# Kernel tuning notes

Measured on AMD Instinct MI355X. Metric: run time of the kernel, lower is better.

The kernel has to match this reference:

```python
import jax, jax.numpy as jnp
import numpy as np

D_MODEL = 1024
D_STATE = 16
D_CONV = 4
EXPAND = 2
MLP_EXPAND = 2
D_INNER = EXPAND * D_MODEL          # 2048
DT_RANK = (D_MODEL + 15) // 16      # 64
BATCH, SEQ = 2, 1024


def setup_inputs() -> dict:
    key = jax.random.key(0)
    ks = jax.random.split(key, 16)
    s = 0.02
    inp = {
        "x": jax.random.normal(ks[0], (BATCH, SEQ, D_MODEL), jnp.float32),
        "norm1_g": jnp.ones((D_MODEL,), jnp.float32),
        "norm1_b": jnp.zeros((D_MODEL,), jnp.float32),
        "in_proj_w": jax.random.normal(ks[1], (2 * D_INNER, D_MODEL), jnp.float32) * s,
        "conv_w": jax.random.normal(ks[2], (D_INNER, 1, D_CONV), jnp.float32) * s,
        "conv_b": jnp.zeros((D_INNER,), jnp.float32),
        "x_proj_w": jax.random.normal(ks[3], (DT_RANK + 2 * D_STATE, D_INNER), jnp.float32) * s,
        "dt_proj_w": jax.random.normal(ks[4], (D_INNER, DT_RANK), jnp.float32) * s,
        "dt_proj_b": jax.random.normal(ks[5], (D_INNER,), jnp.float32) * 0.1,
        "A_log": jnp.log(jnp.broadcast_to(jnp.arange(1, D_STATE + 1, dtype=jnp.float32), (D_INNER, D_STATE))),
        "D_param": jnp.ones((D_INNER,), jnp.float32),
        "out_proj_w": jax.random.normal(ks[6], (D_MODEL, D_INNER), jnp.float32) * s,
        "norm2_g": jnp.ones((D_MODEL,), jnp.float32),
        "norm2_b": jnp.zeros((D_MODEL,), jnp.float32),
        "mlp_w1": jax.random.normal(ks[7], (MLP_EXPAND * D_MODEL, D_MODEL), jnp.float32) * s,
        "mlp_b1": jnp.zeros((MLP_EXPAND * D_MODEL,), jnp.float32),
        "mlp_w2": jax.random.normal(ks[8], (D_MODEL, MLP_EXPAND * D_MODEL), jnp.float32) * s,
        "mlp_b2": jnp.zeros((D_MODEL,), jnp.float32),
    }
    return inp


def _layernorm(x, g, b, eps=1e-5):
    m = jnp.mean(x, axis=-1, keepdims=True)
    v = jnp.var(x, axis=-1, keepdims=True)
    return (x - m) * jax.lax.rsqrt(v + eps) * g + b


def _silu(x):
    return x * jax.nn.sigmoid(x)


def _mamba(x, in_proj_w, conv_w, conv_b, x_proj_w, dt_proj_w, dt_proj_b, A_log, D_param, out_proj_w):
    # x: (B, L, d_model)
    xz = x @ in_proj_w.T                              # (B, L, 2*Di)
    xc, z = jnp.split(xz, 2, axis=-1)                 # each (B, L, Di)
    # causal depthwise conv over time
    xc_t = xc.transpose(0, 2, 1)                      # (B, Di, L)
    xc_t = jax.lax.conv_general_dilated(
        xc_t, conv_w, window_strides=(1,), padding=[(D_CONV - 1, 0)],
        dimension_numbers=("NCH", "OIH", "NCH"), feature_group_count=D_INNER,
    ) + conv_b[None, :, None]
    xc = _silu(xc_t).transpose(0, 2, 1)               # (B, L, Di)

    dbc = xc @ x_proj_w.T                             # (B, L, dt_rank + 2N)
    dt, Bm, Cm = jnp.split(dbc, [DT_RANK, DT_RANK + D_STATE], axis=-1)
    dt = jax.nn.softplus(dt @ dt_proj_w.T + dt_proj_b)  # (B, L, Di)
    A = -jnp.exp(A_log)                               # (Di, N)

    def step(h, inp):
        dt_t, B_t, C_t, x_t = inp                     # (B,Di),(B,N),(B,N),(B,Di)
        dA = jnp.exp(dt_t[..., None] * A)             # (B, Di, N)
        h = dA * h + (dt_t * x_t)[..., None] * B_t[:, None, :]
        y = jnp.einsum("bdn,bn->bd", h, C_t)
        return h, y

    h0 = jnp.zeros((x.shape[0], D_INNER, D_STATE), x.dtype)
    xs = (dt.transpose(1, 0, 2), Bm.transpose(1, 0, 2), Cm.transpose(1, 0, 2), xc.transpose(1, 0, 2))
    _, ys = jax.lax.scan(step, h0, xs)                # ys: (L, B, Di)
    y = ys.transpose(1, 0, 2) + xc * D_param          # skip term D*x
    y = y * _silu(z)
    return y @ out_proj_w.T                           # (B, L, d_model)


def reference(x, norm1_g, norm1_b, in_proj_w, conv_w, conv_b, x_proj_w, dt_proj_w,
              dt_proj_b, A_log, D_param, out_proj_w, norm2_g, norm2_b,
              mlp_w1, mlp_b1, mlp_w2, mlp_b2):
    # residual + Mamba(LN(x))  (droppath=0 -> identity)
    h = x + _mamba(_layernorm(x, norm1_g, norm1_b), in_proj_w, conv_w, conv_b,
                   x_proj_w, dt_proj_w, dt_proj_b, A_log, D_param, out_proj_w)
    # residual + MLP(LN(h))    (dropout eval -> identity)
    m = _layernorm(h, norm2_g, norm2_b)
    m = jax.nn.gelu(m @ mlp_w1.T + mlp_b1, approximate=False) @ mlp_w2.T + mlp_b2
    return h + m
```

## Files before the change

### kernel.cpp

```cpp
#include <hip/hip_runtime.h>
#include <math.h>

#define D_MODEL 1024
#define D_INNER 2048
#define DT_RANK 64
#define D_STATE 16
#define NBC 96
#define BATCH 2
#define SEQ 1024
#define TOK (BATCH*SEQ)
#define CS 32
#define NCH 32
#define XKSPLIT 16

typedef __attribute__((ext_vector_type(8))) short short8;
typedef __attribute__((ext_vector_type(4))) float f32x4;

__device__ __forceinline__ float softplus_f(float x) {
    return (x > 20.0f) ? x : log1pf(__expf(x));
}
__device__ __forceinline__ float gelu_f(float x) {
    return 0.5f * x * (1.0f + erff(x * 0.70710678118654752f));
}
__device__ __forceinline__ float silu_f(float x) {
    return x / (1.0f + __expf(-x));
}
__device__ __forceinline__ ushort f2bf(float f) {
    unsigned u = __float_as_uint(f);
    unsigned r = (u + 0x7fffu + ((u >> 16) & 1u)) >> 16;
    return (ushort)r;
}
__device__ __forceinline__ float bf2f(ushort u) {
    return __uint_as_float(((unsigned)u) << 16);
}

__global__ void convert_weights_kernel(const float* __restrict__ Wp, const float* __restrict__ Wo,
                                       const float* __restrict__ W1, const float* __restrict__ W2,
                                       const float* __restrict__ Wx, const float* __restrict__ Wdt,
                                       ushort* __restrict__ Wpb, ushort* __restrict__ Wob,
                                       ushort* __restrict__ W1b, ushort* __restrict__ W2b,
                                       ushort* __restrict__ Wxb, ushort* __restrict__ Wdtb) {
    int i = blockIdx.x * 256 + threadIdx.x;
    const float* src; ushort* dst; int off;
    if      (i < 1048576) { src = Wp;  dst = Wpb;  off = i; }
    else if (i < 1572864) { src = Wo;  dst = Wob;  off = i - 1048576; }
    else if (i < 2097152) { src = W1;  dst = W1b;  off = i - 1572864; }
    else if (i < 2621440) { src = W2;  dst = W2b;  off = i - 2097152; }
    else if (i < 2670592) { src = Wx;  dst = Wxb;  off = i - 2621440; }
    else if (i < 2703360) { src = Wdt; dst = Wdtb; off = i - 2670592; }
    else return;
    float4 v = ((const float4*)src)[off];
    ushort4 o;
    o.x = f2bf(v.x); o.y = f2bf(v.y); o.z = f2bf(v.z); o.w = f2bf(v.w);
    ((ushort4*)dst)[off] = o;
}

__global__ void ln_bf16_kernel(const float* __restrict__ x, const float* __restrict__ g,
                               const float* __restrict__ b, ushort* __restrict__ out) {
    int row = blockIdx.x;
    const float* xr = x + (size_t)row * D_MODEL;
    ushort* outr = out + (size_t)row * D_MODEL;
    int tid = threadIdx.x;
    float4 v = ((const float4*)xr)[tid];
    float s  = v.x + v.y + v.z + v.w;
    float sq = v.x*v.x + v.y*v.y + v.z*v.z + v.w*v.w;
    #pragma unroll
    for (int o = 32; o > 0; o >>= 1) {
        s  += __shfl_down(s,  o);
        sq += __shfl_down(sq, o);
    }
    __shared__ float ss[4], ssq[4];
    int wid = tid >> 6, lane = tid & 63;
    if (lane == 0) { ss[wid] = s; ssq[wid] = sq; }
    __syncthreads();
    if (tid == 0) {
        float a = 0.f, c = 0.f;
        for (int i = 0; i < 4; i++) { a += ss[i]; c += ssq[i]; }
        ss[0] = a; ssq[0] = c;
    }
    __syncthreads();
    float mean = ss[0] * (1.0f / D_MODEL);
    float var  = ssq[0] * (1.0f / D_MODEL) - mean * mean;
    float rstd = rsqrtf(var + 1e-5f);
    float4 gg = ((const float4*)g)[tid];
    float4 bb = ((const float4*)b)[tid];
    ushort4 o;
    o.x = f2bf((v.x - mean) * rstd * gg.x + bb.x);
    o.y = f2bf((v.y - mean) * rstd * gg.y + bb.y);
    o.z = f2bf((v.z - mean) * rstd * gg.z + bb.z);
    o.w = f2bf((v.w - mean) * rstd * gg.w + bb.w);
    ((ushort4*)outr)[tid] = o;
}

template<int BM, int BN, int ACT, bool BIAS, bool RES, bool OUTBF>
__global__ __launch_bounds__(256)
void mfma_gemm(const ushort* __restrict__ A, const ushort* __restrict__ W,
               const float* __restrict__ bias,
               const float* __restrict__ res, int ldr,
               void* __restrict__ Cout, int ldc, int K) {
    constexpr int WM = BM / 2, WN = BN / 2, FM = WM / 16, FN = WN / 16;
    __shared__ __align__(16) ushort As[BM * 32];
    __shared__ __align__(16) ushort Ws[BN * 32];
    const int tid  = threadIdx.x;
    const int lane = tid & 63, w = tid >> 6;
    const int wr = w >> 1, wc = w & 1;
    const int row0 = blockIdx.y * BM, col0 = blockIdx.x * BN;
    const int l16 = lane >> 4, l15 = lane & 15;
    const int srow = tid >> 2;
    const int scol = (tid & 3) * 8;

    f32x4 acc[FM][FN] = {};

    for (int k0 = 0; k0 < K; k0 += 32) {
        #pragma unroll
        for (int s = 0; s < BM / 64; s++) {
            const ushort* g = A + (size_t)(row0 + s * 64 + srow) * K + k0 + scol;
            __builtin_amdgcn_global_load_lds(
                (const __attribute__((address_space(1))) void*)g,
                (__attribute__((address_space(3))) void*)((char*)As + s * 4096 + w * 1024),
                16, 0, 0);
        }
        #pragma unroll
        for (int s = 0; s < BN / 64; s++) {
            const ushort* g = W + (size_t)(col0 + s * 64 + srow) * K + k0 + scol;
            __builtin_amdgcn_global_load_lds(
                (const __attribute__((address_space(1))) void*)g,
                (__attribute__((address_space(3))) void*)((char*)Ws + s * 4096 + w * 1024),
                16, 0, 0);
        }
        __syncthreads();

        short8 a[FM], b[FN];
        #pragma unroll
        for (int m = 0; m < FM; m++)
            a[m] = *(const short8*)(As + (wr * WM + m * 16 + l15) * 32 + l16 * 8);
        #pragma unroll
        for (int n = 0; n < FN; n++)
            b[n] = *(const short8*)(Ws + (wc * WN + n * 16 + l15) * 32 + l16 * 8);
        #pragma unroll
        for (int m = 0; m < FM; m++)
            #pragma unroll
            for (int n = 0; n < FN; n++)
                acc[m][n] = __builtin_amdgcn_mfma_f32_16x16x32_bf16(a[m], b[n], acc[m][n], 0, 0, 0);
        __syncthreads();
    }

    #pragma unroll
    for (int m = 0; m < FM; m++) {
        const int r0 = row0 + wr * WM + m * 16 + l16 * 4;
        #pragma unroll
        for (int n = 0; n < FN; n++) {
            const int c = col0 + wc * WN + n * 16 + l15;
            const float bv = BIAS ? bias[c] : 0.f;
            #pragma unroll
            for (int q = 0; q < 4; q++) {
                const int r = r0 + q;
                float v = acc[m][n][q] + bv;
                if (ACT == 1) v = softplus_f(v);
                else if (ACT == 2) v = gelu_f(v);
                if (RES) v += res[(size_t)r * ldr + c];
                if (OUTBF) ((ushort*)Cout)[(size_t)r * ldc + c] = f2bf(v);
                else       ((float*)Cout)[(size_t)r * ldc + c] = v;
            }
        }
    }
}

__global__ __launch_bounds__(256)
void xproj_split_kernel(const ushort* __restrict__ A,
                        const ushort* __restrict__ W,
                        float* __restrict__ part) {
    __shared__ __align__(16) ushort As[128 * 64];
    __shared__ __align__(16) ushort Bs[96 * 64];
    const int tid = threadIdx.x;
    const int lane = tid & 63, w = tid >> 6;
    const int l16 = lane >> 4, l15 = lane & 15;
    const int kbase = blockIdx.x * (D_INNER / XKSPLIT);
    const int row0 = blockIdx.y * 128;
    const int srow = tid >> 3;
    const int scol = (tid & 7) * 8;

    f32x4 acc[2][6] = {};

    for (int k0 = 0; k0 < D_INNER / XKSPLIT; k0 += 64) {
        #pragma unroll
        for (int s = 0; s < 4; s++) {
            const ushort* g = A + (size_t)(row0 + s * 32 + srow) * D_INNER + kbase + k0 + scol;
            __builtin_amdgcn_global_load_lds(
                (const __attribute__((address_space(1))) void*)g,
                (__attribute__((address_space(3))) void*)((char*)As + s * 4096 + w * 1024),
                16, 0, 0);
        }
        #pragma unroll
        for (int s = 0; s < 3; s++) {
            const ushort* g = W + (size_t)(s * 32 + srow) * D_INNER + kbase + k0 + scol;
            __builtin_amdgcn_global_load_lds(
                (const __attribute__((address_space(1))) void*)g,
                (__attribute__((address_space(3))) void*)((char*)Bs + s * 4096 + w * 1024),
                16, 0, 0);
        }
        __syncthreads();
        #pragma unroll
        for (int ks = 0; ks < 2; ks++) {
            short8 a[2], b[6];
            #pragma unroll
            for (int m = 0; m < 2; m++)
                a[m] = *(const short8*)(As + (w * 32 + m * 16 + l15) * 64 + ks * 32 + l16 * 8);
            #pragma unroll
            for (int n = 0; n < 6; n++)
                b[n] = *(const short8*)(Bs + (n * 16 + l15) * 64 + ks * 32 + l16 * 8);
            #pragma unroll
            for (int m = 0; m < 2; m++)
                #pragma unroll
                for (int n = 0; n < 6; n++)
                    acc[m][n] = __builtin_amdgcn_mfma_f32_16x16x32_bf16(a[m], b[n], acc[m][n], 0, 0, 0);
        }
        __syncthreads();
    }

    float* p = part + (size_t)blockIdx.x * D_INNER * NBC;
    #pragma unroll
    for (int m = 0; m < 2; m++) {
        const int r0 = row0 + w * 32 + m * 16 + l16 * 4;
        #pragma unroll
        for (int n = 0; n < 6; n++) {
            const int c = n * 16 + l15;
            #pragma unroll
            for (int q = 0; q < 4; q++)
                p[(size_t)(r0 + q) * NBC + c] = acc[m][n][q];
        }
    }
}

__global__ void xproj_reduce_kernel(const float* __restrict__ part,
                                    float* __restrict__ dbc, ushort* __restrict__ dtin_b) {
    int i = blockIdx.x * 256 + threadIdx.x;
    if (i >= D_INNER * NBC) return;
    float s = 0.f;
    #pragma unroll
    for (int k = 0; k < XKSPLIT; k++) s += part[(size_t)k * D_INNER * NBC + i];
    dbc[i] = s;
    int r = i / NBC, c = i - r * NBC;
    if (c < DT_RANK) dtin_b[r * DT_RANK + c] = f2bf(s);
}

__global__ void conv_silu_kernel(const ushort* __restrict__ xzb, const float* __restrict__ cw,
                                 const float* __restrict__ cb, ushort* __restrict__ xcb) {
    int idx = blockIdx.x * 256 + threadIdx.x;
    int c  = idx & (D_INNER - 1);
    int bt = idx >> 11;
    int b  = bt >> 10;
    int t  = bt & (SEQ - 1);
    float acc = cb[c];
    #pragma unroll
    for (int j = 0; j < 4; j++) {
        int tt = t - 3 + j;
        if (tt >= 0) acc += cw[c*4 + j] * bf2f(xzb[((size_t)(b*SEQ + tt)) * 4096 + c]);
    }
    xcb[idx] = f2bf(silu_f(acc));
}

__global__ void scan_chunk_kernel(const float* __restrict__ dt, const float* __restrict__ dbc,
                                  const ushort* __restrict__ xcb, const float* __restrict__ A_log,
                                  float* __restrict__ chunkA, float* __restrict__ chunkH) {
    int idx = blockIdx.x * 256 + threadIdx.x;
    int ng = idx & 3;
    int d  = (idx >> 2) & (D_INNER - 1);
    int r  = idx >> 13;
    int c  = r & (NCH - 1);
    int b  = r >> 5;
    const int nb = ng * 4;
    float Arow[4];
    #pragma unroll
    for (int j = 0; j < 4; j++) Arow[j] = -__expf(A_log[d * D_STATE + nb + j]);
    float h[4] = {};
    float ap[4] = {1.f, 1.f, 1.f, 1.f};
    const size_t rbase = (size_t)(b * SEQ + c * CS);
    for (int t = 0; t < CS; t++) {
        size_t row = rbase + t;
        float dtv = dt[row * D_INNER + d];
        float xv  = bf2f(xcb[row * D_INNER + d]);
        const float* bc = dbc + row * NBC + DT_RANK;
        float dtx = dtv * xv;
        #pragma unroll
        for (int j = 0; j < 4; j++) {
            float dA = __expf(dtv * Arow[j]);
            ap[j] *= dA;
            h[j] = dA * h[j] + dtx * bc[nb + j];
        }
    }
    size_t obase = ((size_t)(b * NCH + c) * D_STATE + nb) * D_INNER + d;
    #pragma unroll
    for (int j = 0; j < 4; j++) {
        chunkA[obase + (size_t)j * D_INNER] = ap[j];
        chunkH[obase + (size_t)j * D_INNER] = h[j];
    }
}

__global__ void scan_combine_kernel(const float* __restrict__ chunkA, float* __restrict__ chunkH) {
    int idx = blockIdx.x * 256 + threadIdx.x;
    int d = idx & (D_INNER - 1);
    int r = idx >> 11;
    int n = r & (D_STATE - 1);
    int b = r >> 4;
    float h = 0.f;
    for (int c = 0; c < NCH; c++) {
        size_t o = ((size_t)((b * NCH + c) * D_STATE + n)) * D_INNER + d;
        float a  = chunkA[o];
        float hl = chunkH[o];
        chunkH[o] = h;
        h = a * h + hl;
    }
}

__global__ void scan_final_kernel(const float* __restrict__ dt, const float* __restrict__ dbc,
                                  const ushort* __restrict__ xcb, const float* __restrict__ A_log,
                                  const float* __restrict__ chunkH, const ushort* __restrict__ xzb,
                                  const float* __restrict__ Dp, ushort* __restrict__ yb) {
    int idx = blockIdx.x * 256 + threadIdx.x;
    int ng = idx & 3;
    int d  = (idx >> 2) & (D_INNER - 1);
    int r  = idx >> 13;
    int c  = r & (NCH - 1);
    int b  = r >> 5;
    const int nb = ng * 4;
    float Arow[4];
    #pragma unroll
    for (int j = 0; j < 4; j++) Arow[j] = -__expf(A_log[d * D_STATE + nb + j]);
    float h[4];
    size_t obase = ((size_t)(b * NCH + c) * D_STATE + nb) * D_INNER + d;
    #pragma unroll
    for (int j = 0; j < 4; j++) h[j] = chunkH[obase + (size_t)j * D_INNER];
    const float Dpv = Dp[d];
    const size_t rbase = (size_t)(b * SEQ + c * CS);
    for (int t = 0; t < CS; t++) {
        size_t row = rbase + t;
        float dtv = dt[row * D_INNER + d];
        float xv  = bf2f(xcb[row * D_INNER + d]);
        const float* bc = dbc + row * NBC + DT_RANK;
        float dtx = dtv * xv;
        float yv = 0.f;
        #pragma unroll
        for (int j = 0; j < 4; j++) {
            float dA = __expf(dtv * Arow[j]);
            h[j] = dA * h[j] + dtx * bc[nb + j];
            yv += h[j] * bc[D_STATE + nb + j];
        }
        yv += __shfl_xor(yv, 1);
        yv += __shfl_xor(yv, 2);
        if (ng == 0) {
            float z = bf2f(xzb[row * 4096 + 2048 + d]);
            yb[row * D_INNER + d] = f2bf((yv + xv * Dpv) * silu_f(z));
        }
    }
}

extern "C" void kernel_launch(void* const* d_in, const int* in_sizes, int n_in,
                              void* d_out, int out_size, void* d_ws, size_t ws_size,
                              hipStream_t stream) {
    const float* x    = (const float*)d_in[0];
    const float* n1g  = (const float*)d_in[1];
    const float* n1b  = (const float*)d_in[2];
    const float* Wp   = (const float*)d_in[3];
    const float* cw   = (const float*)d_in[4];
    const float* cb   = (const float*)d_in[5];
    const float* Wx   = (const float*)d_in[6];
    const float* Wdt  = (const float*)d_in[7];
    const float* bdt  = (const float*)d_in[8];
    const float* Alog = (const float*)d_in[9];
    const float* Dp   = (const float*)d_in[10];
    const float* Wo   = (const float*)d_in[11];
    const float* n2g  = (const float*)d_in[12];
    const float* n2b  = (const float*)d_in[13];
    const float* W1   = (const float*)d_in[14];
    const float* b1   = (const float*)d_in[15];
    const float* W2   = (const float*)d_in[16];
    const float* b2   = (const float*)d_in[17];
    float* out = (float*)d_out;
    float* ws  = (float*)d_ws;

    const size_t M1 = 1024 * 1024;
    ushort* xzb   = (ushort*)ws;
    ushort* xcb   = (ushort*)(ws + 8*M1);
    float*  dtb   = ws + 10*M1;
    float*  part  = ws + 14*M1;
    float*  hbuf  = ws + 14*M1;
    float*  dbc   = ws + 18*M1;
    ushort* dtin_b= (ushort*)(ws + 18*M1 + 262144);
    ushort* xnb   = (ushort*)(ws + 18*M1 + 524288);
    ushort* mb    = xnb;
    ushort* yb    = (ushort*)(ws + 20*M1);
    ushort* t1b   = yb;
    ushort* Wpb   = (ushort*)(ws + 22*M1);
    float*  chunkA= ws + 22*M1;
    ushort* Wob   = (ushort*)(ws + 24*M1);
    ushort* W1b   = (ushort*)(ws + 25*M1);
    ushort* W2b   = (ushort*)(ws + 26*M1);
    ushort* Wxb   = (ushort*)(ws + 27*M1);
    ushort* Wdtb  = (ushort*)(ws + 27*M1 + 131072);
    float*  chunkH = out;

    convert_weights_kernel<<<(2703360 + 255)/256, 256, 0, stream>>>(
        Wp, Wo, W1, W2, Wx, Wdt, Wpb, Wob, W1b, W2b, Wxb, Wdtb);

    ln_bf16_kernel<<<TOK, 256, 0, stream>>>(x, n1g, n1b, xnb);
    mfma_gemm<128,128,0,false,false,true><<<dim3(4096/128, 2048/128), 256, 0, stream>>>(
        xnb, Wpb, nullptr, nullptr, 0, xzb, 2*D_INNER, D_MODEL);
    conv_silu_kernel<<<TOK*D_INNER/256, 256, 0, stream>>>(xzb, cw, cb, xcb);
    xproj_split_kernel<<<dim3(XKSPLIT, 2048/128), 256, 0, stream>>>(xcb, Wxb, part);
    xproj_reduce_kernel<<<(D_INNER*NBC + 255)/256, 256, 0, stream>>>(part, dbc, dtin_b);
    mfma_gemm<128,128,1,true,false,false><<<dim3(2048/128, 2048/128), 256, 0, stream>>>(
        dtin_b, Wdtb, bdt, nullptr, 0, dtb, D_INNER, DT_RANK);
    scan_chunk_kernel<<<BATCH*NCH*D_INNER*4/256, 256, 0, stream>>>(dtb, dbc, xcb, Alog, chunkA, chunkH);
    scan_combine_kernel<<<BATCH*D_STATE*D_INNER/256, 256, 0, stream>>>(chunkA, chunkH);
    scan_final_kernel<<<BATCH*NCH*D_INNER*4/256, 256, 0, stream>>>(dtb, dbc, xcb, Alog, chunkH,
                                                                   xzb, Dp, yb);
    mfma_gemm<128,64,0,false,true,false><<<dim3(1024/64, 2048/128), 256, 0, stream>>>(
        yb, Wob, nullptr, x, D_MODEL, hbuf, D_MODEL, D_INNER);
    ln_bf16_kernel<<<TOK, 256, 0, stream>>>(hbuf, n2g, n2b, mb);
    mfma_gemm<128,128,2,true,false,true><<<dim3(2048/128, 2048/128), 256, 0, stream>>>(
        mb, W1b, b1, nullptr, 0, t1b, D_INNER, D_MODEL);
    mfma_gemm<128,64,0,true,true,false><<<dim3(1024/64, 2048/128), 256, 0, stream>>>(
        t1b, W2b, b2, hbuf, D_MODEL, out, D_MODEL, D_INNER);
}
```

Measured before the change: 270.3 us.

## Store scan inputs time-major per channel for vectorized contiguous scan loads

Switches the scan operands (dt, B/C, conv output, z, y) to a channel-major, time-contiguous layout. GEMM epilogues write dt and z transposed, xproj partials are written transposed, and two bf16 transpose kernels convert xc and y between layouts. The scan kernels then load four timesteps at once as vectors instead of strided per-token loads. The cost is two extra transpose passes and scattered transposed stores in the GEMM epilogues.

New measurement: 340.8 us. +26.1%, slower.

```diff
diff --git a/kernel.cpp b/kernel.cpp
--- a/kernel.cpp
+++ b/kernel.cpp
@@ -15,6 +15,7 @@
 
 typedef __attribute__((ext_vector_type(8))) short short8;
 typedef __attribute__((ext_vector_type(4))) float f32x4;
+typedef __attribute__((ext_vector_type(4))) unsigned short us4;
 
 __device__ __forceinline__ float softplus_f(float x) {
     return (x > 20.0f) ? x : log1pf(__expf(x));
@@ -92,12 +93,12 @@
     ((ushort4*)outr)[tid] = o;
 }
 
-template<int BM, int BN, int ACT, bool BIAS, bool RES, bool OUTBF>
+template<int BM, int BN, int ACT, bool BIAS, bool RES, int OUTMODE>
 __global__ __launch_bounds__(256)
 void mfma_gemm(const ushort* __restrict__ A, const ushort* __restrict__ W,
                const float* __restrict__ bias,
                const float* __restrict__ res, int ldr,
-               void* __restrict__ Cout, int ldc, int K) {
+               void* __restrict__ Cout, void* __restrict__ Cout2, int ldc, int K) {
     constexpr int WM = BM / 2, WN = BN / 2, FM = WM / 16, FN = WN / 16;
     __shared__ __align__(16) ushort As[BM * 32];
     __shared__ __align__(16) ushort Ws[BN * 32];
@@ -152,15 +153,34 @@
         for (int n = 0; n < FN; n++) {
             const int c = col0 + wc * WN + n * 16 + l15;
             const float bv = BIAS ? bias[c] : 0.f;
+            float v[4];
             #pragma unroll
             for (int q = 0; q < 4; q++) {
-                const int r = r0 + q;
-                float v = acc[m][n][q] + bv;
-                if (ACT == 1) v = softplus_f(v);
-                else if (ACT == 2) v = gelu_f(v);
-                if (RES) v += res[(size_t)r * ldr + c];
-                if (OUTBF) ((ushort*)Cout)[(size_t)r * ldc + c] = f2bf(v);
-                else       ((float*)Cout)[(size_t)r * ldc + c] = v;
+                v[q] = acc[m][n][q] + bv;
+                if (ACT == 1) v[q] = softplus_f(v[q]);
+                else if (ACT == 2) v[q] = gelu_f(v[q]);
+                if (RES) v[q] += res[(size_t)(r0 + q) * ldr + c];
+            }
+            if (OUTMODE == 0) {
+                #pragma unroll
+                for (int q = 0; q < 4; q++)
+                    ((float*)Cout)[(size_t)(r0 + q) * ldc + c] = v[q];
+            } else if (OUTMODE == 1) {
+                #pragma unroll
+                for (int q = 0; q < 4; q++)
+                    ((ushort*)Cout)[(size_t)(r0 + q) * ldc + c] = f2bf(v[q]);
+            } else if (OUTMODE == 2) {
+                f32x4 p; p[0] = v[0]; p[1] = v[1]; p[2] = v[2]; p[3] = v[3];
+                *(f32x4*)((float*)Cout + (size_t)c * ldc + r0) = p;
+            } else {
+                if (c < D_INNER) {
+                    #pragma unroll
+                    for (int q = 0; q < 4; q++)
+                        ((ushort*)Cout)[(size_t)(r0 + q) * D_INNER + c] = f2bf(v[q]);
+                } else {
+                    us4 p; p[0] = f2bf(v[0]); p[1] = f2bf(v[1]); p[2] = f2bf(v[2]); p[3] = f2bf(v[3]);
+                    *(us4*)((ushort*)Cout2 + (size_t)(c - D_INNER) * TOK + r0) = p;
+                }
             }
         }
     }
@@ -218,33 +238,31 @@
         __syncthreads();
     }
 
-    float* p = part + (size_t)blockIdx.x * D_INNER * NBC;
+    float* p = part + (size_t)blockIdx.x * NBC * TOK;
     #pragma unroll
     for (int m = 0; m < 2; m++) {
         const int r0 = row0 + w * 32 + m * 16 + l16 * 4;
         #pragma unroll
         for (int n = 0; n < 6; n++) {
             const int c = n * 16 + l15;
-            #pragma unroll
-            for (int q = 0; q < 4; q++)
-                p[(size_t)(r0 + q) * NBC + c] = acc[m][n][q];
+            *(f32x4*)(p + (size_t)c * TOK + r0) = acc[m][n];
         }
     }
 }
 
 __global__ void xproj_reduce_kernel(const float* __restrict__ part,
-                                    float* __restrict__ dbc, ushort* __restrict__ dtin_b) {
+                                    float* __restrict__ dbcT, ushort* __restrict__ dtin_b) {
     int i = blockIdx.x * 256 + threadIdx.x;
-    if (i >= D_INNER * NBC) return;
+    if (i >= NBC * TOK) return;
     float s = 0.f;
     #pragma unroll
-    for (int k = 0; k < XKSPLIT; k++) s += part[(size_t)k * D_INNER * NBC + i];
-    dbc[i] = s;
-    int r = i / NBC, c = i - r * NBC;
-    if (c < DT_RANK) dtin_b[r * DT_RANK + c] = f2bf(s);
-}
-
-__global__ void conv_silu_kernel(const ushort* __restrict__ xzb, const float* __restrict__ cw,
+    for (int k = 0; k < XKSPLIT; k++) s += part[(size_t)k * NBC * TOK + i];
+    dbcT[i] = s;
+    int n = i >> 11, row = i & (TOK - 1);
+    if (n < DT_RANK) dtin_b[row * DT_RANK + n] = f2bf(s);
+}
+
+__global__ void conv_silu_kernel(const ushort* __restrict__ xprec, const float* __restrict__ cw,
                                  const float* __restrict__ cb, ushort* __restrict__ xcb) {
     int idx = blockIdx.x * 256 + threadIdx.x;
     int c  = idx & (D_INNER - 1);
@@ -255,13 +273,31 @@
     #pragma unroll
     for (int j = 0; j < 4; j++) {
         int tt = t - 3 + j;
-        if (tt >= 0) acc += cw[c*4 + j] * bf2f(xzb[((size_t)(b*SEQ + tt)) * 4096 + c]);
+        if (tt >= 0) acc += cw[c*4 + j] * bf2f(xprec[((size_t)(b*SEQ + tt)) * D_INNER + c]);
     }
     xcb[idx] = f2bf(silu_f(acc));
 }
 
-__global__ void scan_chunk_kernel(const float* __restrict__ dt, const float* __restrict__ dbc,
-                                  const ushort* __restrict__ xcb, const float* __restrict__ A_log,
+__global__ __launch_bounds__(256)
+void transpose_bf16_kernel(const ushort* __restrict__ in, ushort* __restrict__ out) {
+    __shared__ ushort tile[64][68];
+    const int tx = threadIdx.x & 63, ty = threadIdx.x >> 6;
+    const int r0 = blockIdx.y * 64, c0 = blockIdx.x * 64;
+    #pragma unroll
+    for (int i = 0; i < 16; i++) {
+        int rr = ty * 16 + i;
+        tile[rr][tx] = in[(size_t)(r0 + rr) * TOK + c0 + tx];
+    }
+    __syncthreads();
+    #pragma unroll
+    for (int i = 0; i < 16; i++) {
+        int rr = ty * 16 + i;
+        out[(size_t)(c0 + rr) * TOK + r0 + tx] = tile[tx][rr];
+    }
+}
+
+__global__ void scan_chunk_kernel(const float* __restrict__ dtT, const float* __restrict__ dbcT,
+                                  const ushort* __restrict__ xcbT, const float* __restrict__ A_log,
                                   float* __restrict__ chunkA, float* __restrict__ chunkH) {
     int idx = blockIdx.x * 256 + threadIdx.x;
     int ng = idx & 3;
@@ -273,20 +309,29 @@
     float Arow[4];
     #pragma unroll
     for (int j = 0; j < 4; j++) Arow[j] = -__expf(A_log[d * D_STATE + nb + j]);
+    const int rbase = b * SEQ + c * CS;
+    const float*  pdt = dtT  + (size_t)d * TOK + rbase;
+    const ushort* pxv = xcbT + (size_t)d * TOK + rbase;
+    const float*  pB  = dbcT + (size_t)(DT_RANK + nb) * TOK + rbase;
+    const float*  pC  = dbcT + (size_t)(DT_RANK + D_STATE + nb) * TOK + rbase;
     float h[4] = {};
     float ap[4] = {1.f, 1.f, 1.f, 1.f};
-    const size_t rbase = (size_t)(b * SEQ + c * CS);
-    for (int t = 0; t < CS; t++) {
-        size_t row = rbase + t;
-        float dtv = dt[row * D_INNER + d];
-        float xv  = bf2f(xcb[row * D_INNER + d]);
-        const float* bc = dbc + row * NBC + DT_RANK;
-        float dtx = dtv * xv;
-        #pragma unroll
-        for (int j = 0; j < 4; j++) {
-            float dA = __expf(dtv * Arow[j]);
-            ap[j] *= dA;
-            h[j] = dA * h[j] + dtx * bc[nb + j];
+    for (int it = 0; it < CS / 4; ++it) {
+        f32x4 dt4 = *(const f32x4*)(pdt + it * 4);
+        us4   xu  = *(const us4*)(pxv + it * 4);
+        f32x4 Bv[4];
+        #pragma unroll
+        for (int j = 0; j < 4; j++) Bv[j] = *(const f32x4*)(pB + (size_t)j * TOK + it * 4);
+        #pragma unroll
+        for (int q = 0; q < 4; ++q) {
+            float dtv = dt4[q];
+            float dtx = dtv * bf2f(xu[q]);
+            #pragma unroll
+            for (int j = 0; j < 4; j++) {
+                float dA = __expf(dtv * Arow[j]);
+                ap[j] *= dA;
+                h[j] = dA * h[j] + dtx * Bv[j][q];
+            }
         }
     }
     size_t obase = ((size_t)(b * NCH + c) * D_STATE + nb) * D_INNER + d;
@@ -313,10 +358,10 @@
     }
 }
 
-__global__ void scan_final_kernel(const float* __restrict__ dt, const float* __restrict__ dbc,
-                                  const ushort* __restrict__ xcb, const float* __restrict__ A_log,
-                                  const float* __restrict__ chunkH, const ushort* __restrict__ xzb,
-                                  const float* __restrict__ Dp, ushort* __restrict__ yb) {
+__global__ void scan_final_kernel(const float* __restrict__ dtT, const float* __restrict__ dbcT,
+                                  const ushort* __restrict__ xcbT, const float* __restrict__ A_log,
+                                  const float* __restrict__ chunkH, const ushort* __restrict__ zT,
+                                  const float* __restrict__ Dp, ushort* __restrict__ ybT) {
     int idx = blockIdx.x * 256 + threadIdx.x;
     int ng = idx & 3;
     int d  = (idx >> 2) & (D_INNER - 1);
@@ -332,25 +377,50 @@
     #pragma unroll
     for (int j = 0; j < 4; j++) h[j] = chunkH[obase + (size_t)j * D_INNER];
     const float Dpv = Dp[d];
-    const size_t rbase = (size_t)(b * SEQ + c * CS);
-    for (int t = 0; t < CS; t++) {
-        size_t row = rbase + t;
-        float dtv = dt[row * D_INNER + d];
-        float xv  = bf2f(xcb[row * D_INNER + d]);
-        const float* bc = dbc + row * NBC + DT_RANK;
-        float dtx = dtv * xv;
-        float yv = 0.f;
+    const int rbase = b * SEQ + c * CS;
+    const float*  pdt = dtT  + (size_t)d * TOK + rbase;
+    const ushort* pxv = xcbT + (size_t)d * TOK + rbase;
+    const ushort* pz  = zT   + (size_t)d * TOK + rbase;
+    const float*  pB  = dbcT + (size_t)(DT_RANK + nb) * TOK + rbase;
+    const float*  pC  = dbcT + (size_t)(DT_RANK + D_STATE + nb) * TOK + rbase;
+    ushort*       py  = ybT  + (size_t)d * TOK + rbase;
+    for (int it = 0; it < CS / 4; ++it) {
+        f32x4 dt4 = *(const f32x4*)(pdt + it * 4);
+        us4   xu  = *(const us4*)(pxv + it * 4);
+        f32x4 Bv[4], Cv[4];
         #pragma unroll
         for (int j = 0; j < 4; j++) {
-            float dA = __expf(dtv * Arow[j]);
-            h[j] = dA * h[j] + dtx * bc[nb + j];
-            yv += h[j] * bc[D_STATE + nb + j];
-        }
-        yv += __shfl_xor(yv, 1);
-        yv += __shfl_xor(yv, 2);
+            Bv[j] = *(const f32x4*)(pB + (size_t)j * TOK + it * 4);
+            Cv[j] = *(const f32x4*)(pC + (size_t)j * TOK + it * 4);
+        }
+        float yv4[4];
+        #pragma unroll
+        for (int q = 0; q < 4; ++q) {
+            float dtv = dt4[q];
+            float dtx = dtv * bf2f(xu[q]);
+            float yv = 0.f;
+            #pragma unroll
+            for (int j = 0; j < 4; j++) {
+                float dA = __expf(dtv * Arow[j]);
+                h[j] = dA * h[j] + dtx * Bv[j][q];
+                yv += h[j] * Cv[j][q];
+            }
+            yv4[q] = yv;
+        }
+        #pragma unroll
+        for (int q = 0; q < 4; ++q) {
+            yv4[q] += __shfl_xor(yv4[q], 1);
+            yv4[q] += __shfl_xor(yv4[q], 2);
+        }
         if (ng == 0) {
-            float z = bf2f(xzb[row * 4096 + 2048 + d]);
-            yb[row * D_INNER + d] = f2bf((yv + xv * Dpv) * silu_f(z));
+            us4 zu = *(const us4*)(pz + it * 4);
+            us4 o;
+            #pragma unroll
+            for (int q = 0; q < 4; ++q) {
+                float z = bf2f(zu[q]);
+                o[q] = f2bf((yv4[q] + bf2f(xu[q]) * Dpv) * silu_f(z));
+            }
+            *(us4*)(py + it * 4) = o;
         }
     }
 }
@@ -380,46 +450,51 @@
     float* ws  = (float*)d_ws;
 
     const size_t M1 = 1024 * 1024;
-    ushort* xzb   = (ushort*)ws;
-    ushort* xcb   = (ushort*)(ws + 8*M1);
-    float*  dtb   = ws + 10*M1;
-    float*  part  = ws + 14*M1;
-    float*  hbuf  = ws + 14*M1;
-    float*  dbc   = ws + 18*M1;
-    ushort* dtin_b= (ushort*)(ws + 18*M1 + 262144);
-    ushort* xnb   = (ushort*)(ws + 18*M1 + 524288);
+    ushort* xprec = (ushort*)ws;
+    ushort* zT    = (ushort*)(ws + 2*M1);
+    ushort* xcb   = (ushort*)(ws + 4*M1);
+    ushort* xcbT  = (ushort*)(ws + 6*M1);
+    float*  dtT   = ws + 8*M1;
+    float*  part  = ws + 12*M1;
+    float*  hbuf  = ws + 12*M1;
+    float*  dbcT  = ws + 15*M1;
+    ushort* dtin_b= (ushort*)(ws + 15*M1 + 262144);
+    ushort* xnb   = (ushort*)(ws + 15*M1 + 524288);
     ushort* mb    = xnb;
-    ushort* yb    = (ushort*)(ws + 20*M1);
+    ushort* ybT   = (ushort*)(ws + 17*M1);
+    ushort* yb    = (ushort*)(ws + 19*M1);
     ushort* t1b   = yb;
-    ushort* Wpb   = (ushort*)(ws + 22*M1);
-    float*  chunkA= ws + 22*M1;
-    ushort* Wob   = (ushort*)(ws + 24*M1);
-    ushort* W1b   = (ushort*)(ws + 25*M1);
-    ushort* W2b   = (ushort*)(ws + 26*M1);
-    ushort* Wxb   = (ushort*)(ws + 27*M1);
-    ushort* Wdtb  = (ushort*)(ws + 27*M1 + 131072);
+    ushort* Wpb   = (ushort*)(ws + 21*M1);
+    float*  chunkA= ws + 21*M1;
+    ushort* Wob   = (ushort*)(ws + 23*M1);
+    ushort* W1b   = (ushort*)(ws + 24*M1);
+    ushort* W2b   = (ushort*)(ws + 25*M1);
+    ushort* Wxb   = (ushort*)(ws + 26*M1);
+    ushort* Wdtb  = (ushort*)(ws + 26*M1 + 131072);
     float*  chunkH = out;
 
     convert_weights_kernel<<<(2703360 + 255)/256, 256, 0, stream>>>(
         Wp, Wo, W1, W2, Wx, Wdt, Wpb, Wob, W1b, W2b, Wxb, Wdtb);
 
     ln_bf16_kernel<<<TOK, 256, 0, stream>>>(x, n1g, n1b, xnb);
-    mfma_gemm<128,128,0,false,false,true><<<dim3(4096/128, 2048/128), 256, 0, stream>>>(
-        xnb, Wpb, nullptr, nullptr, 0, xzb, 2*D_INNER, D_MODEL);
-    conv_silu_kernel<<<TOK*D_INNER/256, 256, 0, stream>>>(xzb, cw, cb, xcb);
+    mfma_gemm<128,128,0,false,false,3><<<dim3(4096/128, 2048/128), 256, 0, stream>>>(
+        xnb, Wpb, nullptr, nullptr, 0, xprec, zT, D_INNER, D_MODEL);
+    conv_silu_kernel<<<TOK*D_INNER/256, 256, 0, stream>>>(xprec, cw, cb, xcb);
+    transpose_bf16_kernel<<<dim3(32,32), 256, 0, stream>>>(xcb, xcbT);
     xproj_split_kernel<<<dim3(XKSPLIT, 2048/128), 256, 0, stream>>>(xcb, Wxb, part);
-    xproj_reduce_kernel<<<(D_INNER*NBC + 255)/256, 256, 0, stream>>>(part, dbc, dtin_b);
-    mfma_gemm<128,128,1,true,false,false><<<dim3(2048/128, 2048/128), 256, 0, stream>>>(
-        dtin_b, Wdtb, bdt, nullptr, 0, dtb, D_INNER, DT_RANK);
-    scan_chunk_kernel<<<BATCH*NCH*D_INNER*4/256, 256, 0, stream>>>(dtb, dbc, xcb, Alog, chunkA, chunkH);
+    xproj_reduce_kernel<<<(NBC*TOK + 255)/256, 256, 0, stream>>>(part, dbcT, dtin_b);
+    mfma_gemm<128,128,1,true,false,2><<<dim3(2048/128, 2048/128), 256, 0, stream>>>(
+        dtin_b, Wdtb, bdt, nullptr, 0, dtT, nullptr, TOK, DT_RANK);
+    scan_chunk_kernel<<<BATCH*NCH*D_INNER*4/256, 256, 0, stream>>>(dtT, dbcT, xcbT, Alog, chunkA, chunkH);
     scan_combine_kernel<<<BATCH*D_STATE*D_INNER/256, 256, 0, stream>>>(chunkA, chunkH);
-    scan_final_kernel<<<BATCH*NCH*D_INNER*4/256, 256, 0, stream>>>(dtb, dbc, xcb, Alog, chunkH,
-                                                                   xzb, Dp, yb);
-    mfma_gemm<128,64,0,false,true,false><<<dim3(1024/64, 2048/128), 256, 0, stream>>>(
-        yb, Wob, nullptr, x, D_MODEL, hbuf, D_MODEL, D_INNER);
+    scan_final_kernel<<<BATCH*NCH*D_INNER*4/256, 256, 0, stream>>>(dtT, dbcT, xcbT, Alog, chunkH,
+                                                                   zT, Dp, ybT);
+    transpose_bf16_kernel<<<dim3(32,32), 256, 0, stream>>>(ybT, yb);
+    mfma_gemm<128,64,0,false,true,0><<<dim3(1024/64, 2048/128), 256, 0, stream>>>(
+        yb, Wob, nullptr, x, D_MODEL, hbuf, nullptr, D_MODEL, D_INNER);
     ln_bf16_kernel<<<TOK, 256, 0, stream>>>(hbuf, n2g, n2b, mb);
-    mfma_gemm<128,128,2,true,false,true><<<dim3(2048/128, 2048/128), 256, 0, stream>>>(
-        mb, W1b, b1, nullptr, 0, t1b, D_INNER, D_MODEL);
-    mfma_gemm<128,64,0,true,true,false><<<dim3(1024/64, 2048/128), 256, 0, stream>>>(
-        t1b, W2b, b2, hbuf, D_MODEL, out, D_MODEL, D_INNER);
-}
+    mfma_gemm<128,128,2,true,false,1><<<dim3(2048/128, 2048/128), 256, 0, stream>>>(
+        mb, W1b, b1, nullptr, 0, t1b, nullptr, D_INNER, D_MODEL);
+    mfma_gemm<128,64,0,true,true,0><<<dim3(1024/64, 2048/128), 256, 0, stream>>>(
+        t1b, W2b, b2, hbuf, D_MODEL, out, nullptr, D_MODEL, D_INNER);
+}
```

## Stage scan chunk inputs in LDS and batch per-timestep loads and stores

Applied to the files above, without the earlier changes.

The chunk scan and final scan kernels now have each block cooperatively load a 64-channel by 32-timestep tile of dt, x, z and the B/C values into shared memory. Each thread then reads its time series from LDS as 4-wide vectors, and the final kernel stages its bf16 outputs in LDS and writes them back row-coalesced. Before, each thread issued serial global loads every timestep with poor coalescing (stride of 4 lanes per channel) and repeatedly read B/C. The cost is extra shared memory, a block barrier, and padded LDS layouts that may cause bank conflicts.

Result: no change. 267.3 us (-1.1%).

```diff
diff --git a/kernel.cpp b/kernel.cpp
--- a/kernel.cpp
+++ b/kernel.cpp
@@ -15,6 +15,7 @@
 
 typedef __attribute__((ext_vector_type(8))) short short8;
 typedef __attribute__((ext_vector_type(4))) float f32x4;
+typedef __attribute__((ext_vector_type(4))) unsigned short us4;
 
 __device__ __forceinline__ float softplus_f(float x) {
     return (x > 20.0f) ? x : log1pf(__expf(x));
@@ -260,36 +261,61 @@
     xcb[idx] = f2bf(silu_f(acc));
 }
 
-__global__ void scan_chunk_kernel(const float* __restrict__ dt, const float* __restrict__ dbc,
-                                  const ushort* __restrict__ xcb, const float* __restrict__ A_log,
-                                  float* __restrict__ chunkA, float* __restrict__ chunkH) {
-    int idx = blockIdx.x * 256 + threadIdx.x;
-    int ng = idx & 3;
-    int d  = (idx >> 2) & (D_INNER - 1);
-    int r  = idx >> 13;
-    int c  = r & (NCH - 1);
-    int b  = r >> 5;
-    const int nb = ng * 4;
+__global__ __launch_bounds__(256)
+void scan_chunk_kernel(const float* __restrict__ dtb, const float* __restrict__ dbc,
+                       const ushort* __restrict__ xcb, const float* __restrict__ A_log,
+                       float* __restrict__ chunkA, float* __restrict__ chunkH) {
+    __shared__ float  dtS[64][36];
+    __shared__ ushort xS[64][36];
+    __shared__ float  BS[16][36];
+    const int bid = blockIdx.x;
+    const int dg = bid & 31, cc = (bid >> 5) & 31, b = bid >> 10;
+    const int d0 = dg * 64;
+    const int tid = threadIdx.x, lane = tid & 63, wv = tid >> 6;
+    const int rbase = b * SEQ + cc * CS;
+
+    #pragma unroll
+    for (int k = 0; k < 8; k++) {
+        int tt = k * 4 + wv;
+        size_t row = (size_t)(rbase + tt);
+        dtS[lane][tt] = dtb[row * D_INNER + d0 + lane];
+        xS[lane][tt]  = xcb[row * D_INNER + d0 + lane];
+    }
+    #pragma unroll
+    for (int k = 0; k < 2; k++) {
+        int ii = k * 256 + tid;
+        int val = ii & 15, tt = ii >> 4;
+        BS[val][tt] = dbc[(size_t)(rbase + tt) * NBC + DT_RANK + val];
+    }
+    __syncthreads();
+
+    const int d_local = tid >> 2, ng = tid & 3, nb = ng * 4;
+    const int d = d0 + d_local;
     float Arow[4];
     #pragma unroll
     for (int j = 0; j < 4; j++) Arow[j] = -__expf(A_log[d * D_STATE + nb + j]);
     float h[4] = {};
     float ap[4] = {1.f, 1.f, 1.f, 1.f};
-    const size_t rbase = (size_t)(b * SEQ + c * CS);
-    for (int t = 0; t < CS; t++) {
-        size_t row = rbase + t;
-        float dtv = dt[row * D_INNER + d];
-        float xv  = bf2f(xcb[row * D_INNER + d]);
-        const float* bc = dbc + row * NBC + DT_RANK;
-        float dtx = dtv * xv;
-        #pragma unroll
-        for (int j = 0; j < 4; j++) {
-            float dA = __expf(dtv * Arow[j]);
-            ap[j] *= dA;
-            h[j] = dA * h[j] + dtx * bc[nb + j];
-        }
-    }
-    size_t obase = ((size_t)(b * NCH + c) * D_STATE + nb) * D_INNER + d;
+    #pragma unroll
+    for (int it = 0; it < 8; ++it) {
+        f32x4 dt4 = *(const f32x4*)&dtS[d_local][it * 4];
+        us4   xu  = *(const us4*)&xS[d_local][it * 4];
+        f32x4 Bv[4];
+        #pragma unroll
+        for (int j = 0; j < 4; j++) Bv[j] = *(const f32x4*)&BS[nb + j][it * 4];
+        #pragma unroll
+        for (int q = 0; q < 4; ++q) {
+            float dtv = dt4[q];
+            float dtx = dtv * bf2f(xu[q]);
+            #pragma unroll
+            for (int j = 0; j < 4; j++) {
+                float dA = __expf(dtv * Arow[j]);
+                ap[j] *= dA;
+                h[j] = dA * h[j] + dtx * Bv[j][q];
+            }
+        }
+    }
+    size_t obase = ((size_t)((b * NCH + cc) * D_STATE) + nb) * D_INNER + d;
     #pragma unroll
     for (int j = 0; j < 4; j++) {
         chunkA[obase + (size_t)j * D_INNER] = ap[j];
@@ -313,45 +339,98 @@
     }
 }
 
-__global__ void scan_final_kernel(const float* __restrict__ dt, const float* __restrict__ dbc,
-                                  const ushort* __restrict__ xcb, const float* __restrict__ A_log,
-                                  const float* __restrict__ chunkH, const ushort* __restrict__ xzb,
-                                  const float* __restrict__ Dp, ushort* __restrict__ yb) {
-    int idx = blockIdx.x * 256 + threadIdx.x;
-    int ng = idx & 3;
-    int d  = (idx >> 2) & (D_INNER - 1);
-    int r  = idx >> 13;
-    int c  = r & (NCH - 1);
-    int b  = r >> 5;
-    const int nb = ng * 4;
+__global__ __launch_bounds__(256)
+void scan_final_kernel(const float* __restrict__ dtb, const float* __restrict__ dbc,
+                       const ushort* __restrict__ xcb, const float* __restrict__ A_log,
+                       const float* __restrict__ chunkH, const ushort* __restrict__ xzb,
+                       const float* __restrict__ Dp, ushort* __restrict__ yb) {
+    __shared__ float  dtS[64][36];
+    __shared__ ushort xS[64][36];
+    __shared__ ushort zS[64][36];
+    __shared__ float  BS[16][36];
+    __shared__ float  CSld[16][36];
+    __shared__ ushort ySt[64][36];
+    const int bid = blockIdx.x;
+    const int dg = bid & 31, cc = (bid >> 5) & 31, b = bid >> 10;
+    const int d0 = dg * 64;
+    const int tid = threadIdx.x, lane = tid & 63, wv = tid >> 6;
+    const int rbase = b * SEQ + cc * CS;
+
+    #pragma unroll
+    for (int k = 0; k < 8; k++) {
+        int tt = k * 4 + wv;
+        size_t row = (size_t)(rbase + tt);
+        dtS[lane][tt] = dtb[row * D_INNER + d0 + lane];
+        xS[lane][tt]  = xcb[row * D_INNER + d0 + lane];
+        zS[lane][tt]  = xzb[row * 4096 + 2048 + d0 + lane];
+    }
+    #pragma unroll
+    for (int k = 0; k < 4; k++) {
+        int ii = k * 256 + tid;
+        int val = ii & 31, tt = ii >> 5;
+        float v = dbc[(size_t)(rbase + tt) * NBC + DT_RANK + val];
+        if (val < 16) BS[val][tt] = v;
+        else          CSld[val - 16][tt] = v;
+    }
+    __syncthreads();
+
+    const int d_local = tid >> 2, ng = tid & 3, nb = ng * 4;
+    const int d = d0 + d_local;
     float Arow[4];
     #pragma unroll
     for (int j = 0; j < 4; j++) Arow[j] = -__expf(A_log[d * D_STATE + nb + j]);
     float h[4];
-    size_t obase = ((size_t)(b * NCH + c) * D_STATE + nb) * D_INNER + d;
+    size_t obase = ((size_t)((b * NCH + cc) * D_STATE) + nb) * D_INNER + d;
     #pragma unroll
     for (int j = 0; j < 4; j++) h[j] = chunkH[obase + (size_t)j * D_INNER];
     const float Dpv = Dp[d];
-    const size_t rbase = (size_t)(b * SEQ + c * CS);
-    for (int t = 0; t < CS; t++) {
-        size_t row = rbase + t;
-        float dtv = dt[row * D_INNER + d];
-        float xv  = bf2f(xcb[row * D_INNER + d]);
-        const float* bc = dbc + row * NBC + DT_RANK;
-        float dtx = dtv * xv;
-        float yv = 0.f;
+
+    #pragma unroll
+    for (int it = 0; it < 8; ++it) {
+        f32x4 dt4 = *(const f32x4*)&dtS[d_local][it * 4];
+        us4   xu  = *(const us4*)&xS[d_local][it * 4];
+        f32x4 Bv[4], Cv[4];
         #pragma unroll
         for (int j = 0; j < 4; j++) {
-            float dA = __expf(dtv * Arow[j]);
-            h[j] = dA * h[j] + dtx * bc[nb + j];
-            yv += h[j] * bc[D_STATE + nb + j];
-        }
-        yv += __shfl_xor(yv, 1);
-        yv += __shfl_xor(yv, 2);
+            Bv[j] = *(const f32x4*)&BS[nb + j][it * 4];
+            Cv[j] = *(const f32x4*)&CSld[nb + j][it * 4];
+        }
+        float yv4[4];
+        #pragma unroll
+        for (int q = 0; q < 4; ++q) {
+            float dtv = dt4[q];
+            float dtx = dtv * bf2f(xu[q]);
+            float yv = 0.f;
+            #pragma unroll
+            for (int j = 0; j < 4; j++) {
+                float dA = __expf(dtv * Arow[j]);
+                h[j] = dA * h[j] + dtx * Bv[j][q];
+                yv += h[j] * Cv[j][q];
+            }
+            yv4[q] = yv;
+        }
+        #pragma unroll
+        for (int q = 0; q < 4; ++q) {
+            yv4[q] += __shfl_xor(yv4[q], 1);
+            yv4[q] += __shfl_xor(yv4[q], 2);
+        }
         if (ng == 0) {
-            float z = bf2f(xzb[row * 4096 + 2048 + d]);
-            yb[row * D_INNER + d] = f2bf((yv + xv * Dpv) * silu_f(z));
-        }
+            us4 zu = *(const us4*)&zS[d_local][it * 4];
+            us4 xo = *(const us4*)&xS[d_local][it * 4];
+            us4 o;
+            #pragma unroll
+            for (int q = 0; q < 4; ++q) {
+                float z = bf2f(zu[q]);
+                o[q] = f2bf((yv4[q] + bf2f(xo[q]) * Dpv) * silu_f(z));
+            }
+            *(us4*)&ySt[d_local][it * 4] = o;
+        }
+    }
+    __syncthreads();
+    #pragma unroll
+    for (int k = 0; k < 8; k++) {
+        int tt = k * 4 + wv;
+        yb[(size_t)(rbase + tt) * D_INNER + d0 + lane] = ySt[lane][tt];
     }
 }
 
@@ -411,10 +490,10 @@
     xproj_reduce_kernel<<<(D_INNER*NBC + 255)/256, 256, 0, stream>>>(part, dbc, dtin_b);
     mfma_gemm<128,128,1,true,false,false><<<dim3(2048/128, 2048/128), 256, 0, stream>>>(
         dtin_b, Wdtb, bdt, nullptr, 0, dtb, D_INNER, DT_RANK);
-    scan_chunk_kernel<<<BATCH*NCH*D_INNER*4/256, 256, 0, stream>>>(dtb, dbc, xcb, Alog, chunkA, chunkH);
+    scan_chunk_kernel<<<BATCH*NCH*(D_INNER/64), 256, 0, stream>>>(dtb, dbc, xcb, Alog, chunkA, chunkH);
     scan_combine_kernel<<<BATCH*D_STATE*D_INNER/256, 256, 0, stream>>>(chunkA, chunkH);
-    scan_final_kernel<<<BATCH*NCH*D_INNER*4/256, 256, 0, stream>>>(dtb, dbc, xcb, Alog, chunkH,
-                                                                   xzb, Dp, yb);
+    scan_final_kernel<<<BATCH*NCH*(D_INNER/64), 256, 0, stream>>>(dtb, dbc, xcb, Alog, chunkH,
+                                                                  xzb, Dp, yb);
     mfma_gemm<128,64,0,false,true,false><<<dim3(1024/64, 2048/128), 256, 0, stream>>>(
         yb, Wob, nullptr, x, D_MODEL, hbuf, D_MODEL, D_INNER);
     ln_bf16_kernel<<<TOK, 256, 0, stream>>>(hbuf, n2g, n2b, mb);
```
